# Kernel optimization log

Measured on AMD Instinct MI355X. Metric: run time of the kernel, lower is better.

The kernel has to match this reference:

```python
import jax, jax.numpy as jnp
import numpy as np
from jax import lax

WIN = 9  # window side length (default [9]*ndims in the torch module)


def _box_sum3d(x, win):
    # x: [C, 1, D, H, W]; sliding-window sum with zero padding == conv3d with
    return lax.reduce_window(
        x, jnp.array(0, x.dtype), lax.add,
        window_dimensions=(1, 1, win, win, win),
        window_strides=(1, 1, 1, 1, 1),
        padding='SAME')


def setup_inputs() -> dict:
    key = jax.random.key(0)
    k1, k2 = jax.random.split(key)
    shape = (1, 2, 192, 224, 192)  # [batch, channel, D, H, W]
    y_pred = jax.random.uniform(k1, shape, dtype=jnp.float32)
    y_true = jax.random.uniform(k2, shape, dtype=jnp.float32)
    return {"y_pred": y_pred, "y_true": y_true}


def reference(y_pred, y_true):
    # permute(1, 0, 2, 3, 4): [B, C, D, H, W] -> [C, B, D, H, W]
    Ii = jnp.transpose(y_pred, (1, 0, 2, 3, 4))
    Ji = jnp.transpose(y_true, (1, 0, 2, 3, 4))
    win_size = jnp.array(WIN ** 3, Ii.dtype)

    I_sum = _box_sum3d(Ii, WIN)
    J_sum = _box_sum3d(Ji, WIN)
    I2_sum = _box_sum3d(Ii * Ii, WIN)
    J2_sum = _box_sum3d(Ji * Ji, WIN)
    IJ_sum = _box_sum3d(Ii * Ji, WIN)

    u_I = I_sum / win_size
    u_J = J_sum / win_size

    cross = IJ_sum - u_J * I_sum - u_I * J_sum + u_I * u_J * win_size
    I_var = I2_sum - 2 * u_I * I_sum + u_I * u_I * win_size
    J_var = J2_sum - 2 * u_J * J_sum + u_J * u_J * win_size

    cc = cross * cross / (I_var * J_var + 1e-5)
    return -jnp.mean(cc)
```

## Files before the change

### kernel.cpp

```cpp
#include <hip/hip_runtime.h>
#include <hip/hip_fp16.h>


#define C2   2
#define DDIM 192
#define HDIM 224
#define WDIM 192
#define HWN  (HDIM*WDIM)
#define VOL  ((size_t)DDIM*HWN)
#define RAD  4
#define WINV (1.0f/729.0f)

#define HT1  28
#define NROW 200

__global__ __launch_bounds__(192)
void k_hwsum(const float* __restrict__ I, const float* __restrict__ J,
             __half* __restrict__ buf, int d0, int dbeg, int dend, int bufD)
{
    const int tx = threadIdx.x;
    const int s  = tx / 96;
    const int p  = tx % 96;
    const int w0 = 2 * p;
    int d = dbeg + 2*blockIdx.x + s;
    if (d >= dend) d = dend - 1;
    const int h0 = blockIdx.y * HT1;
    const int c  = blockIdx.z;

    __shared__ float row[2][2][5][NROW];

    for (int t = tx; t < 2*2*5*8; t += 192) {
        const int k    = t & 7;
        const int rest = t >> 3;
        const int pos  = (k < 4) ? k : (192 + k);
        (&row[0][0][0][0])[rest*NROW + pos] = 0.f;
    }
    __syncthreads();

    const float* Ib = I + (size_t)c*VOL + (size_t)d*HWN + w0;
    const float* Jb = J + (size_t)c*VOL + (size_t)d*HWN + w0;

    float2 ring[5][9];
    float2 rs[5];
    #pragma unroll
    for (int f = 0; f < 5; ++f) { rs[f].x = 0.f; rs[f].y = 0.f; }

    #pragma unroll
    for (int k = 0; k < 8; ++k) {
        const int h = h0 - RAD + k;
        float2 iv = {0.f,0.f}, jv = {0.f,0.f};
        if (h >= 0 && h < HDIM) {
            iv = *(const float2*)(Ib + (size_t)h*WDIM);
            jv = *(const float2*)(Jb + (size_t)h*WDIM);
        }
        float2 pr[5];
        pr[0] = iv; pr[1] = jv;
        pr[2].x = iv.x*iv.x; pr[2].y = iv.y*iv.y;
        pr[3].x = jv.x*jv.x; pr[3].y = jv.y*jv.y;
        pr[4].x = iv.x*jv.x; pr[4].y = iv.y*jv.y;
        #pragma unroll
        for (int f = 0; f < 5; ++f) {
            ring[f][k] = pr[f];
            rs[f].x += pr[f].x; rs[f].y += pr[f].y;
        }
    }

    float2 niv = {0.f,0.f}, njv = {0.f,0.f};
    {
        const int hf = h0 + RAD;
        if (hf < HDIM) {
            niv = *(const float2*)(Ib + (size_t)hf*WDIM);
            njv = *(const float2*)(Jb + (size_t)hf*WDIM);
        }
    }

    const size_t fstride = (size_t)C2*bufD*HWN;
    __half* ob = buf + ((size_t)c*bufD + (size_t)(d - d0 + RAD))*HWN + w0;

    int i = 0;
    while (i < HT1) {
        #pragma unroll
        for (int p9 = 0; p9 < 9; ++p9) {
            if (i < HT1) {
                const int h = h0 + i;
                const float2 iv = niv, jv = njv;
                niv.x = 0.f; niv.y = 0.f; njv.x = 0.f; njv.y = 0.f;
                const int hf2 = h + 1 + RAD;
                if (i + 1 < HT1 && hf2 < HDIM) {
                    niv = *(const float2*)(Ib + (size_t)hf2*WDIM);
                    njv = *(const float2*)(Jb + (size_t)hf2*WDIM);
                }
                float2 pr[5];
                pr[0] = iv; pr[1] = jv;
                pr[2].x = iv.x*iv.x; pr[2].y = iv.y*iv.y;
                pr[3].x = jv.x*jv.x; pr[3].y = jv.y*jv.y;
                pr[4].x = iv.x*jv.x; pr[4].y = iv.y*jv.y;
                float* rb = &row[s][h & 1][0][0];
                #pragma unroll
                for (int f = 0; f < 5; ++f) {
                    rs[f].x += pr[f].x; rs[f].y += pr[f].y;
                    *(float2*)(rb + f*NROW + 4 + w0) = rs[f];
                    rs[f].x -= ring[f][p9].x; rs[f].y -= ring[f][p9].y;
                    ring[f][(p9+8)%9] = pr[f];
                }
                __syncthreads();
                #pragma unroll
                for (int f = 0; f < 5; ++f) {
                    const float* q = rb + f*NROW + w0;
                    const float2 r0 = *(const float2*)(q + 0);
                    const float2 r1 = *(const float2*)(q + 2);
                    const float2 r2 = *(const float2*)(q + 4);
                    const float2 r3 = *(const float2*)(q + 6);
                    const float2 r4 = *(const float2*)(q + 8);
                    const float s9 = r0.x+r0.y+r1.x+r1.y+r2.x+r2.y+r3.x+r3.y+r4.x;
                    const float o0 = s9;
                    const float o1 = s9 - r0.x + r4.y;
                    *reinterpret_cast<__half2*>(ob + f*fstride + (size_t)h*WDIM)
                        = __floats2half2_rn(o0, o1);
                }
                ++i;
            }
        }
    }
}

__global__ __launch_bounds__(256)
void k_dsum(const __half* __restrict__ buf, double* __restrict__ gacc,
            int d0, int bufD, int DS)
{
    const int tid = threadIdx.x;
    const int pix = blockIdx.x*256 + tid;
    const int c   = blockIdx.z;
    const int ds0 = d0 + blockIdx.y*DS;

    const size_t fstride = (size_t)C2*bufD*HWN;
    const __half* base = buf + (size_t)c*bufD*HWN + pix;

    float ring[5][9];
    float rs[5] = {0.f,0.f,0.f,0.f,0.f};
    float acc = 0.f;

    #pragma unroll
    for (int k = 0; k < 8; ++k) {
        const int dd = ds0 - RAD + k;
        float v[5] = {0.f,0.f,0.f,0.f,0.f};
        if ((unsigned)dd < (unsigned)DDIM) {
            const __half* pp = base + (size_t)(dd - d0 + RAD)*HWN;
            #pragma unroll
            for (int f = 0; f < 5; ++f) v[f] = __half2float(pp[(size_t)f*fstride]);
        }
        #pragma unroll
        for (int f = 0; f < 5; ++f) { ring[f][k] = v[f]; rs[f] += v[f]; }
    }

    int i = 0;
    while (i < DS) {
        #pragma unroll
        for (int p = 0; p < 9; ++p) {
            if (i < DS) {
                const int dd = ds0 + i + RAD;
                float v[5] = {0.f,0.f,0.f,0.f,0.f};
                if (dd < DDIM) {
                    const __half* pp = base + (size_t)(dd - d0 + RAD)*HWN;
                    #pragma unroll
                    for (int f = 0; f < 5; ++f) v[f] = __half2float(pp[(size_t)f*fstride]);
                }
                float S[5];
                #pragma unroll
                for (int f = 0; f < 5; ++f) {
                    rs[f] += v[f];
                    S[f] = rs[f];
                    rs[f] -= ring[f][p];
                    ring[f][(p+8)%9] = v[f];
                }
                const float uI    = S[0]*WINV;
                const float uJ    = S[1]*WINV;
                const float cross = S[4] - uJ*S[0];
                const float Iv    = S[2] - uI*S[0];
                const float Jv    = S[3] - uJ*S[1];
                acc += cross*cross / (Iv*Jv + 1e-5f);
                ++i;
            }
        }
    }

    __shared__ float wred[4];
    #pragma unroll
    for (int off = 32; off > 0; off >>= 1) acc += __shfl_down(acc, off);
    if ((tid & 63) == 0) wred[tid >> 6] = acc;
    __syncthreads();
    if (tid == 0) {
        const float sum = wred[0] + wred[1] + wred[2] + wred[3];
        atomicAdd(gacc, (double)sum);
    }
}

__global__ void k_fin(const double* __restrict__ gacc, float* __restrict__ out)
{
    out[0] = (float)(-gacc[0] / (double)((size_t)C2*DDIM*HDIM*WDIM));
}

extern "C" void kernel_launch(void* const* d_in, const int* in_sizes, int n_in,
                              void* d_out, int out_size, void* d_ws, size_t ws_size,
                              hipStream_t stream)
{
    if (n_in < 2) return;
    const float* I = (const float*)d_in[0];
    const float* J = (const float*)d_in[1];
    float* out = (float*)d_out;
    double* gacc = (double*)d_ws;
    __half* buf = (__half*)((char*)d_ws + 256);

    static const int cands[] = {192, 96, 48, 24, 12, 6, 4, 2, 1};
    int Dc = 0;
    for (int c : cands) {
        const size_t need = 256 + (size_t)5*C2*(c+8)*HWN*sizeof(__half);
        if (need <= ws_size) { Dc = c; break; }
    }
    if (Dc == 0) return;

    hipMemsetAsync(d_ws, 0, 256, stream);

    const int DS   = (Dc % 48 == 0) ? 48 : Dc;
    const int nsub = Dc / DS;
    const int bufD = Dc + 8;

    for (int d0 = 0; d0 < DDIM; d0 += Dc) {
        const int dbeg = (d0 - RAD < 0) ? 0 : d0 - RAD;
        const int dend = (d0 + Dc + RAD > DDIM) ? DDIM : d0 + Dc + RAD;
        const int nd   = dend - dbeg;
        dim3 g1((nd + 1)/2, HDIM/HT1, C2);
        k_hwsum<<<g1, dim3(192,1,1), 0, stream>>>(I, J, buf, d0, dbeg, dend, bufD);
        dim3 g2(HWN/256, nsub, C2);
        k_dsum<<<g2, dim3(256,1,1), 0, stream>>>(buf, gacc, d0, bufD, DS);
    }
    k_fin<<<1,1,0,stream>>>(gacc, out);
}
```

Baseline: 118.2 us.

## Reorder separable box sum: depth pass first, then fused H/W pass with CC reduction

Swaps the order of the separable box-filter passes. The first kernel now computes the five products and their running depth sums over the full volume, stored in fp16. The second kernel does the H and W sums in registers, using neighbouring 4-wide loads instead of shared memory and barriers, and fuses the cross-correlation and reduction. This drops the chunked multi-launch loop and the per-row __syncthreads. In exchange it needs a full-volume fp16 workspace and reads overlapping neighbour data redundantly in the W direction.

Measured after the change: 148.4 us. +25.5%, slower.

```diff
diff --git a/kernel.cpp b/kernel.cpp
--- a/kernel.cpp
+++ b/kernel.cpp
@@ -8,37 +8,30 @@
 #define WDIM 192
 #define HWN  (HDIM*WDIM)
 #define VOL  ((size_t)DDIM*HWN)
+#define SVOL ((size_t)DDIM*HWN)
 #define RAD  4
 #define WINV (1.0f/729.0f)
 
-#define HT1  28
-#define NROW 200
-
-__global__ __launch_bounds__(192)
-void k_hwsum(const float* __restrict__ I, const float* __restrict__ J,
-             __half* __restrict__ buf, int d0, int dbeg, int dend, int bufD)
-{
-    const int tx = threadIdx.x;
-    const int s  = tx / 96;
-    const int p  = tx % 96;
-    const int w0 = 2 * p;
-    int d = dbeg + 2*blockIdx.x + s;
-    if (d >= dend) d = dend - 1;
-    const int h0 = blockIdx.y * HT1;
-    const int c  = blockIdx.z;
-
-    __shared__ float row[2][2][5][NROW];
-
-    for (int t = tx; t < 2*2*5*8; t += 192) {
-        const int k    = t & 7;
-        const int rest = t >> 3;
-        const int pos  = (k < 4) ? k : (192 + k);
-        (&row[0][0][0][0])[rest*NROW + pos] = 0.f;
-    }
-    __syncthreads();
-
-    const float* Ib = I + (size_t)c*VOL + (size_t)d*HWN + w0;
-    const float* Jb = J + (size_t)c*VOL + (size_t)d*HWN + w0;
+#define HT2  28
+
+__global__ __launch_bounds__(256)
+void k_dprod(const float* __restrict__ I, const float* __restrict__ J,
+             __half* __restrict__ buf, int DS)
+{
+    const int tid  = threadIdx.x;
+    const int pair = blockIdx.x*256 + tid;
+    const int pix  = 2*pair;
+    const int c    = blockIdx.z;
+    const int ds0  = blockIdx.y*DS;
+
+    const float* Ib = I + (size_t)c*VOL + pix;
+    const float* Jb = J + (size_t)c*VOL + pix;
+
+    __half* ob0 = buf + (size_t)(0*C2 + c)*SVOL + pix;
+    __half* ob1 = buf + (size_t)(1*C2 + c)*SVOL + pix;
+    __half* ob2 = buf + (size_t)(2*C2 + c)*SVOL + pix;
+    __half* ob3 = buf + (size_t)(3*C2 + c)*SVOL + pix;
+    __half* ob4 = buf + (size_t)(4*C2 + c)*SVOL + pix;
 
     float2 ring[5][9];
     float2 rs[5];
@@ -47,11 +40,11 @@
 
     #pragma unroll
     for (int k = 0; k < 8; ++k) {
-        const int h = h0 - RAD + k;
+        const int dd = ds0 - RAD + k;
         float2 iv = {0.f,0.f}, jv = {0.f,0.f};
-        if (h >= 0 && h < HDIM) {
-            iv = *(const float2*)(Ib + (size_t)h*WDIM);
-            jv = *(const float2*)(Jb + (size_t)h*WDIM);
+        if ((unsigned)dd < (unsigned)DDIM) {
+            iv = *(const float2*)(Ib + (size_t)dd*HWN);
+            jv = *(const float2*)(Jb + (size_t)dd*HWN);
         }
         float2 pr[5];
         pr[0] = iv; pr[1] = jv;
@@ -65,58 +58,31 @@
         }
     }
 
-    float2 niv = {0.f,0.f}, njv = {0.f,0.f};
-    {
-        const int hf = h0 + RAD;
-        if (hf < HDIM) {
-            niv = *(const float2*)(Ib + (size_t)hf*WDIM);
-            njv = *(const float2*)(Jb + (size_t)hf*WDIM);
-        }
-    }
-
-    const size_t fstride = (size_t)C2*bufD*HWN;
-    __half* ob = buf + ((size_t)c*bufD + (size_t)(d - d0 + RAD))*HWN + w0;
-
     int i = 0;
-    while (i < HT1) {
-        #pragma unroll
-        for (int p9 = 0; p9 < 9; ++p9) {
-            if (i < HT1) {
-                const int h = h0 + i;
-                const float2 iv = niv, jv = njv;
-                niv.x = 0.f; niv.y = 0.f; njv.x = 0.f; njv.y = 0.f;
-                const int hf2 = h + 1 + RAD;
-                if (i + 1 < HT1 && hf2 < HDIM) {
-                    niv = *(const float2*)(Ib + (size_t)hf2*WDIM);
-                    njv = *(const float2*)(Jb + (size_t)hf2*WDIM);
+    while (i < DS) {
+        #pragma unroll
+        for (int p = 0; p < 9; ++p) {
+            if (i < DS) {
+                const int dd = ds0 + i + RAD;
+                float2 iv = {0.f,0.f}, jv = {0.f,0.f};
+                if (dd < DDIM) {
+                    iv = *(const float2*)(Ib + (size_t)dd*HWN);
+                    jv = *(const float2*)(Jb + (size_t)dd*HWN);
                 }
                 float2 pr[5];
                 pr[0] = iv; pr[1] = jv;
                 pr[2].x = iv.x*iv.x; pr[2].y = iv.y*iv.y;
                 pr[3].x = jv.x*jv.x; pr[3].y = jv.y*jv.y;
                 pr[4].x = iv.x*jv.x; pr[4].y = iv.y*jv.y;
-                float* rb = &row[s][h & 1][0][0];
+                const size_t doff = (size_t)(ds0 + i)*HWN;
                 #pragma unroll
                 for (int f = 0; f < 5; ++f) {
                     rs[f].x += pr[f].x; rs[f].y += pr[f].y;
-                    *(float2*)(rb + f*NROW + 4 + w0) = rs[f];
-                    rs[f].x -= ring[f][p9].x; rs[f].y -= ring[f][p9].y;
-                    ring[f][(p9+8)%9] = pr[f];
-                }
-                __syncthreads();
-                #pragma unroll
-                for (int f = 0; f < 5; ++f) {
-                    const float* q = rb + f*NROW + w0;
-                    const float2 r0 = *(const float2*)(q + 0);
-                    const float2 r1 = *(const float2*)(q + 2);
-                    const float2 r2 = *(const float2*)(q + 4);
-                    const float2 r3 = *(const float2*)(q + 6);
-                    const float2 r4 = *(const float2*)(q + 8);
-                    const float s9 = r0.x+r0.y+r1.x+r1.y+r2.x+r2.y+r3.x+r3.y+r4.x;
-                    const float o0 = s9;
-                    const float o1 = s9 - r0.x + r4.y;
-                    *reinterpret_cast<__half2*>(ob + f*fstride + (size_t)h*WDIM)
-                        = __floats2half2_rn(o0, o1);
+                    const __half2 h2 = __floats2half2_rn(rs[f].x, rs[f].y);
+                    __half* ob = (f==0)?ob0:(f==1)?ob1:(f==2)?ob2:(f==3)?ob3:ob4;
+                    *reinterpret_cast<__half2*>(ob + doff) = h2;
+                    rs[f].x -= ring[f][p].x; rs[f].y -= ring[f][p].y;
+                    ring[f][(p+8)%9] = pr[f];
                 }
                 ++i;
             }
@@ -124,73 +90,123 @@
     }
 }
 
-__global__ __launch_bounds__(256)
-void k_dsum(const __half* __restrict__ buf, double* __restrict__ gacc,
-            int d0, int bufD, int DS)
-{
-    const int tid = threadIdx.x;
-    const int pix = blockIdx.x*256 + tid;
-    const int c   = blockIdx.z;
-    const int ds0 = d0 + blockIdx.y*DS;
-
-    const size_t fstride = (size_t)C2*bufD*HWN;
-    const __half* base = buf + (size_t)c*bufD*HWN + pix;
-
-    float ring[5][9];
-    float rs[5] = {0.f,0.f,0.f,0.f,0.f};
+__global__ __launch_bounds__(192)
+void k_hwcc(const __half* __restrict__ buf, double* __restrict__ gacc)
+{
+    const int tid  = threadIdx.x;
+    const int wg   = tid % 48;
+    const int dloc = tid / 48;
+    const int w0   = 4*wg;
+    const int d    = (int)blockIdx.x*4 + dloc;
+    const int h0   = (int)blockIdx.y*HT2;
+    const int c    = (int)blockIdx.z;
+    const bool le = (wg == 0), re = (wg == 47);
+
+    const __half* B[5];
+    #pragma unroll
+    for (int f = 0; f < 5; ++f)
+        B[f] = buf + (size_t)(f*C2 + c)*SVOL + (size_t)d*HWN + w0;
+
+    float4 L[5], M[5], R[5];
+    #pragma unroll
+    for (int f = 0; f < 5; ++f) {
+        L[f].x=L[f].y=L[f].z=L[f].w=0.f;
+        M[f].x=M[f].y=M[f].z=M[f].w=0.f;
+        R[f].x=R[f].y=R[f].z=R[f].w=0.f;
+    }
+
+#define LOADRAW(H, OK, A)                                                     \
+    {                                                                         \
+        _Pragma("unroll")                                                     \
+        for (int f = 0; f < 5; ++f) {                                         \
+            const __half* rp = B[f] + (size_t)(H)*WDIM;                       \
+            A[f][0].x = A[f][0].y = 0u;                                       \
+            A[f][1].x = A[f][1].y = 0u;                                       \
+            A[f][2].x = A[f][2].y = 0u;                                       \
+            if (OK) {                                                         \
+                A[f][1] = *reinterpret_cast<const uint2*>(rp);                \
+                if (!le) A[f][0] = *reinterpret_cast<const uint2*>(rp - 4);   \
+                if (!re) A[f][2] = *reinterpret_cast<const uint2*>(rp + 4);   \
+            }                                                                 \
+        }                                                                     \
+    }
+
+#define CVT4(U, V)                                                            \
+    {                                                                         \
+        const __half2 h01 = __builtin_bit_cast(__half2, U.x);                 \
+        const __half2 h23 = __builtin_bit_cast(__half2, U.y);                 \
+        const float2 f01 = __half22float2(h01);                               \
+        const float2 f23 = __half22float2(h23);                               \
+        V.x = f01.x; V.y = f01.y; V.z = f23.x; V.w = f23.y;                   \
+    }
+
+    uint2 pa[5][3], da[5][3];
+
+    for (int k = 0; k < 8; ++k) {
+        const int h = h0 - RAD + k;
+        LOADRAW(h, (h >= 0), da);
+        #pragma unroll
+        for (int f = 0; f < 5; ++f) {
+            float4 v;
+            CVT4(da[f][0], v); L[f].x+=v.x; L[f].y+=v.y; L[f].z+=v.z; L[f].w+=v.w;
+            CVT4(da[f][1], v); M[f].x+=v.x; M[f].y+=v.y; M[f].z+=v.z; M[f].w+=v.w;
+            CVT4(da[f][2], v); R[f].x+=v.x; R[f].y+=v.y; R[f].z+=v.z; R[f].w+=v.w;
+        }
+    }
+    LOADRAW(h0 + RAD, true, pa);
+
     float acc = 0.f;
 
-    #pragma unroll
-    for (int k = 0; k < 8; ++k) {
-        const int dd = ds0 - RAD + k;
-        float v[5] = {0.f,0.f,0.f,0.f,0.f};
-        if ((unsigned)dd < (unsigned)DDIM) {
-            const __half* pp = base + (size_t)(dd - d0 + RAD)*HWN;
-            #pragma unroll
-            for (int f = 0; f < 5; ++f) v[f] = __half2float(pp[(size_t)f*fstride]);
-        }
-        #pragma unroll
-        for (int f = 0; f < 5; ++f) { ring[f][k] = v[f]; rs[f] += v[f]; }
-    }
-
-    int i = 0;
-    while (i < DS) {
-        #pragma unroll
-        for (int p = 0; p < 9; ++p) {
-            if (i < DS) {
-                const int dd = ds0 + i + RAD;
-                float v[5] = {0.f,0.f,0.f,0.f,0.f};
-                if (dd < DDIM) {
-                    const __half* pp = base + (size_t)(dd - d0 + RAD)*HWN;
-                    #pragma unroll
-                    for (int f = 0; f < 5; ++f) v[f] = __half2float(pp[(size_t)f*fstride]);
-                }
-                float S[5];
-                #pragma unroll
-                for (int f = 0; f < 5; ++f) {
-                    rs[f] += v[f];
-                    S[f] = rs[f];
-                    rs[f] -= ring[f][p];
-                    ring[f][(p+8)%9] = v[f];
-                }
-                const float uI    = S[0]*WINV;
-                const float uJ    = S[1]*WINV;
-                const float cross = S[4] - uJ*S[0];
-                const float Iv    = S[2] - uI*S[0];
-                const float Jv    = S[3] - uJ*S[1];
-                acc += cross*cross / (Iv*Jv + 1e-5f);
-                ++i;
-            }
-        }
-    }
-
-    __shared__ float wred[4];
+    for (int i = 0; i < HT2; ++i) {
+        const int h = h0 + i;
+        #pragma unroll
+        for (int f = 0; f < 5; ++f) {
+            float4 v;
+            CVT4(pa[f][0], v); L[f].x+=v.x; L[f].y+=v.y; L[f].z+=v.z; L[f].w+=v.w;
+            CVT4(pa[f][1], v); M[f].x+=v.x; M[f].y+=v.y; M[f].z+=v.z; M[f].w+=v.w;
+            CVT4(pa[f][2], v); R[f].x+=v.x; R[f].y+=v.y; R[f].z+=v.z; R[f].w+=v.w;
+        }
+        LOADRAW(h + RAD + 1, (i + 1 < HT2) && (h + RAD + 1 < HDIM), pa);
+        LOADRAW(h - RAD, (h - RAD >= 0), da);
+
+        float o[5][4];
+        #pragma unroll
+        for (int f = 0; f < 5; ++f) {
+            const float o0 = ((L[f].x+L[f].y)+(L[f].z+L[f].w))
+                           + ((M[f].x+M[f].y)+(M[f].z+M[f].w)) + R[f].x;
+            o[f][0] = o0;
+            o[f][1] = o0      - L[f].x + R[f].y;
+            o[f][2] = o[f][1] - L[f].y + R[f].z;
+            o[f][3] = o[f][2] - L[f].z + R[f].w;
+        }
+        #pragma unroll
+        for (int j = 0; j < 4; ++j) {
+            const float uI    = o[0][j]*WINV;
+            const float uJ    = o[1][j]*WINV;
+            const float cross = o[4][j] - uJ*o[0][j];
+            const float Iv    = o[2][j] - uI*o[0][j];
+            const float Jv    = o[3][j] - uJ*o[1][j];
+            acc += cross*cross / (Iv*Jv + 1e-5f);
+        }
+
+        #pragma unroll
+        for (int f = 0; f < 5; ++f) {
+            float4 v;
+            CVT4(da[f][0], v); L[f].x-=v.x; L[f].y-=v.y; L[f].z-=v.z; L[f].w-=v.w;
+            CVT4(da[f][1], v); M[f].x-=v.x; M[f].y-=v.y; M[f].z-=v.z; M[f].w-=v.w;
+            CVT4(da[f][2], v); R[f].x-=v.x; R[f].y-=v.y; R[f].z-=v.z; R[f].w-=v.w;
+        }
+    }
+#undef LOADRAW
+#undef CVT4
+
+    __shared__ float wred[3];
     #pragma unroll
     for (int off = 32; off > 0; off >>= 1) acc += __shfl_down(acc, off);
     if ((tid & 63) == 0) wred[tid >> 6] = acc;
     __syncthreads();
     if (tid == 0) {
-        const float sum = wred[0] + wred[1] + wred[2] + wred[3];
+        const float sum = wred[0] + wred[1] + wred[2];
         atomicAdd(gacc, (double)sum);
     }
 }
@@ -211,28 +227,17 @@
     double* gacc = (double*)d_ws;
     __half* buf = (__half*)((char*)d_ws + 256);
 
-    static const int cands[] = {192, 96, 48, 24, 12, 6, 4, 2, 1};
-    int Dc = 0;
-    for (int c : cands) {
-        const size_t need = 256 + (size_t)5*C2*(c+8)*HWN*sizeof(__half);
-        if (need <= ws_size) { Dc = c; break; }
-    }
-    if (Dc == 0) return;
+    const size_t need = 256 + (size_t)5*C2*SVOL*sizeof(__half);
+    if (need > ws_size) return;
 
     hipMemsetAsync(d_ws, 0, 256, stream);
 
-    const int DS   = (Dc % 48 == 0) ? 48 : Dc;
-    const int nsub = Dc / DS;
-    const int bufD = Dc + 8;
-
-    for (int d0 = 0; d0 < DDIM; d0 += Dc) {
-        const int dbeg = (d0 - RAD < 0) ? 0 : d0 - RAD;
-        const int dend = (d0 + Dc + RAD > DDIM) ? DDIM : d0 + Dc + RAD;
-        const int nd   = dend - dbeg;
-        dim3 g1((nd + 1)/2, HDIM/HT1, C2);
-        k_hwsum<<<g1, dim3(192,1,1), 0, stream>>>(I, J, buf, d0, dbeg, dend, bufD);
-        dim3 g2(HWN/256, nsub, C2);
-        k_dsum<<<g2, dim3(256,1,1), 0, stream>>>(buf, gacc, d0, bufD, DS);
-    }
+    const int DS = 48;
+    dim3 g1(HWN/512, DDIM/DS, C2);
+    k_dprod<<<g1, dim3(256,1,1), 0, stream>>>(I, J, buf, DS);
+
+    dim3 g2(DDIM/4, HDIM/HT2, C2);
+    k_hwcc<<<g2, dim3(192,1,1), 0, stream>>>(buf, gacc);
+
     k_fin<<<1,1,0,stream>>>(gacc, out);
 }
```
